# Kernel tuning notes

Measured on AMD Instinct MI355X. Metric: run time of the kernel, lower is better.

Reference implementation:

```python
import jax, jax.numpy as jnp
import numpy as np

H, E, V = 1024, 8, 32000
B, S = 2, 2048
RANK, ALPHA = 4, 1.0
LORA_SCALE = ALPHA / RANK
TOP_K = 2
C1, DEC = 4096, 256
CACHE_SIZES = np.array([C1 - i * DEC for i in range(E)])  # [4096,...,2304]
CMAX = int(CACHE_SIZES.max())
H2 = H // 2  # pyramid compression ratio 0.5


def setup_inputs() -> dict:
    key = jax.random.key(0)
    ks = jax.random.split(key, 24)
    n = lambda k, shape, s=1.0: jax.random.normal(k, shape, dtype=jnp.float32) * s
    w = 1.0 / np.sqrt(H)
    inp = {
        "x": n(ks[0], (B, S, H)),
        "query": n(ks[1], (B, S, H)),
        "cache_values": n(ks[2], (E, CMAX, H)),
        "cache_importance": jax.random.uniform(ks[3], (E, CMAX), dtype=jnp.float32),
        "Wr": n(ks[4], (H, E), w),
        "Wexp": n(ks[5], (E, H, H), w),
        "bexp": jnp.zeros((E, H), jnp.float32),
        "Aexp": n(ks[6], (E, H, RANK), w),
        "Bexp": n(ks[7], (E, RANK, H), w),
        "Wq": n(ks[8], (H, H), w),
        "bq": jnp.zeros((H,), jnp.float32),
        "Wk": n(ks[9], (H, H), w),
        "bk": jnp.zeros((H,), jnp.float32),
        "Aq": n(ks[10], (H, RANK), w),
        "Bq": n(ks[11], (RANK, H), w),
        "Ak": n(ks[12], (H, RANK), w),
        "Bk": n(ks[13], (RANK, H), w),
        "Wd": n(ks[14], (H, H2), w),
        "Wu": n(ks[15], (H2, H), 1.0 / np.sqrt(H2)),
        "Av": n(ks[16], (E, H, RANK), w),
        "Bv": n(ks[17], (E, RANK, H), w),
        "Wv": n(ks[18], (H, V), w),
        "bv": jnp.zeros((V,), jnp.float32),
    }
    # compressor weights are per-expert in the original (one per KVCache)
    inp["Wd"] = n(ks[19], (E, H, H2), w)
    inp["Wu"] = n(ks[20], (E, H2, H), 1.0 / np.sqrt(H2))
    return inp


def reference(x, query, cache_values, cache_importance, Wr, Wexp, bexp, Aexp, Bexp,
              Wq, bq, Wk, bk, Aq, Bq, Ak, Bk, Wd, Wu, Av, Bv, Wv, bv):
    # ---- AdaptiveRouter: softmax gate, top-2, renormalize, scatter to dense ----
    gate = jax.nn.softmax(jnp.einsum("bsh,he->bse", x, Wr), axis=-1)       # [B,S,E]
    topv, topi = jax.lax.top_k(gate, TOP_K)                                 # [B,S,K]
    topv = topv / jnp.sum(topv, axis=-1, keepdims=True)
    rw = jnp.sum(jax.nn.one_hot(topi, E, dtype=x.dtype) * topv[..., None], axis=-2)  # [B,S,E]

    # ---- compute_token_importance: LoRA-augmented q/k projections + attention ----
    q = query @ Wq + bq + LORA_SCALE * ((query @ Aq) @ Bq)                  # [B,S,H]
    k = x @ Wk + bk + LORA_SCALE * ((x @ Ak) @ Bk)                          # [B,S,H]
    att = jax.nn.softmax(jnp.einsum("bqh,bkh->bqk", q, k) / np.sqrt(H), axis=-1)
    importance = jnp.sum(att, axis=1)                                       # [B,S] (sum over queries)

    # ---- per-expert KV cache: pyramid compress (down-gelu-up, importance gate) + value LoRA, masked mean ----
    valid = jnp.asarray(np.arange(CMAX)[None, :] < CACHE_SIZES[:, None], x.dtype)  # [E,Cmax]
    h = jax.nn.gelu(jnp.einsum("ech,ehd->ecd", cache_values, Wd))           # [E,Cmax,H2]
    comp = jnp.einsum("ecd,edh->ech", h, Wu) * jax.nn.sigmoid(cache_importance)[..., None]
    comp = comp + LORA_SCALE * jnp.einsum("ech,ehr,erd->ecd", comp, Av, Bv)
    cached = jnp.sum(comp * valid[..., None], axis=1) / jnp.asarray(CACHE_SIZES, x.dtype)[:, None]  # [E,H]

    # ---- dense loop over all LoRA experts (original runs every expert on every token) ----
    eo = jnp.einsum("bsh,ehd->bsed", x, Wexp) + bexp                        # [B,S,E,H]
    eo = eo + LORA_SCALE * jnp.einsum("bsh,ehr,erd->bsed", x, Aexp, Bexp)
    eo = eo + cached[None, None]                                            # broadcast cached values
    expert_output = jnp.einsum("bsed,bse->bsd", eo, rw)                     # routed combine

    logits = expert_output @ Wv + bv                                        # [B,S,V]
    return logits, importance
```

## Files before the change

### kernel.cpp

```cpp
#include <hip/hip_runtime.h>

typedef __bf16 bf16_t;
typedef __bf16 bf16x4 __attribute__((ext_vector_type(4)));
typedef __bf16 bf16x8 __attribute__((ext_vector_type(8)));
typedef float f32x4 __attribute__((ext_vector_type(4)));

#define AS1 __attribute__((address_space(1)))
#define AS3 __attribute__((address_space(3)))
#define BAR() asm volatile("s_barrier" ::: "memory")

__device__ __forceinline__ void gload_lds16(const void* g, void* l) {
  __builtin_amdgcn_global_load_lds((AS1 void*)g, (AS3 void*)l, 16, 0, 0);
}

__device__ __forceinline__ void stage_tile(const bf16_t* g, int ld, bf16_t* lds, int tid) {
  int w = tid >> 6, lane = tid & 63;
#pragma unroll
  for (int r = 0; r < 2; ++r) {
    int rowbase = r * 64 + w * 16;
    const bf16_t* gp = g + (long)(rowbase + (lane >> 2)) * ld + (lane & 3) * 8;
    bf16_t* lp = lds + rowbase * 32;
    gload_lds16(gp, lp);
  }
}

__device__ __forceinline__ void gemm_core(const bf16_t* A, const bf16_t* Bt, int lda, int ldb,
                                          int K, int rowBase, int colBase,
                                          bf16_t* As, bf16_t* Bs, f32x4 acc[4][4]) {
  int tid = threadIdx.x;
  int lane = tid & 63, w = tid >> 6;
  int wr = w >> 1, wc = w & 1;
  int lr = lane & 15, kg = lane >> 4;
  const bf16_t* Ab = A + (long)rowBase * lda;
  const bf16_t* Bb = Bt + (long)colBase * ldb;
  for (int kt = 0; kt < K; kt += 32) {
    __syncthreads();
    stage_tile(Ab + kt, lda, As, tid);
    stage_tile(Bb + kt, ldb, Bs, tid);
    __syncthreads();
    bf16x8 a[4], b[4];
#pragma unroll
    for (int m = 0; m < 4; ++m)
      a[m] = *(const bf16x8*)&As[(wr * 64 + m * 16 + lr) * 32 + kg * 8];
#pragma unroll
    for (int n = 0; n < 4; ++n)
      b[n] = *(const bf16x8*)&Bs[(wc * 64 + n * 16 + lr) * 32 + kg * 8];
#pragma unroll
    for (int m = 0; m < 4; ++m)
#pragma unroll
      for (int n = 0; n < 4; ++n)
        acc[m][n] = __builtin_amdgcn_mfma_f32_16x16x32_bf16(a[m], b[n], acc[m][n], 0, 0, 0);
  }
}

__device__ __forceinline__ void zero_acc(f32x4 acc[4][4]) {
#pragma unroll
  for (int m = 0; m < 4; ++m)
#pragma unroll
    for (int n = 0; n < 4; ++n)
#pragma unroll
      for (int i = 0; i < 4; ++i) acc[m][n][i] = 0.f;
}

__device__ __forceinline__ void pipe256(const bf16_t* __restrict__ Ag,
                                        const bf16_t* __restrict__ Bg,
                                        int K, int ntk, bf16_t* lds, f32x4 acc[8][4]) {
  int tid = threadIdx.x;
  int lane = tid & 63, w = tid >> 6;
  int wr = w >> 2, wc = w & 3;
  int lr = lane & 15, kg = lane >> 4;
  int colE = ((lane & 7) ^ (lane >> 3)) * 8;
  int r0 = w * 16 + (lane >> 3);

  auto stageA = [&](int t, int h) {
    const bf16_t* g = Ag + (long)(h * 128 + r0) * K + t * 64 + colE;
    bf16_t* l = lds + (t & 1) * 16384 + h * 8192 + w * 1024;
    gload_lds16(g, l);
    gload_lds16(g + (long)8 * K, l + 512);
  };
  auto stageB = [&](int t, int h) {
    const bf16_t* g = Bg + (long)(h * 128 + r0) * K + t * 64 + colE;
    bf16_t* l = lds + 32768 + (t % 3) * 16384 + h * 8192 + w * 1024;
    gload_lds16(g, l);
    gload_lds16(g + (long)8 * K, l + 512);
  };

  stageB(0, 0); stageB(0, 1); stageA(0, 0); stageA(0, 1);
  if (ntk > 1) { stageB(1, 0); stageB(1, 1); }
  if (ntk > 1) asm volatile("s_waitcnt vmcnt(4)" ::: "memory");
  else         asm volatile("s_waitcnt vmcnt(0)" ::: "memory");
  BAR();

  for (int t = 0; t < ntk; ++t) {
    const bf16_t* Ar = lds + (t & 1) * 16384 + wr * 8192;
    const bf16_t* Br = lds + 32768 + (t % 3) * 16384 + (wc >> 1) * 8192;
    int bRowOff = (wc & 1) * 64;
    bf16x8 bfr[4][2];
#pragma unroll
    for (int p = 0; p < 4; ++p) {
      if (p == 0) {
#pragma unroll
        for (int n = 0; n < 4; ++n) {
          int R = bRowOff + n * 16 + lr;
#pragma unroll
          for (int ks = 0; ks < 2; ++ks)
            bfr[n][ks] = *(const bf16x8*)(Br + R * 64 + ((ks * 4 + kg) ^ (R & 7)) * 8);
        }
      }
      bf16x8 afr[2][2];
#pragma unroll
      for (int mm = 0; mm < 2; ++mm) {
        int R = p * 32 + mm * 16 + lr;
#pragma unroll
        for (int ks = 0; ks < 2; ++ks)
          afr[mm][ks] = *(const bf16x8*)(Ar + R * 64 + ((ks * 4 + kg) ^ (R & 7)) * 8);
      }
      if (p < 2) { if (t + 1 < ntk) stageA(t + 1, p); }
      else       { if (t + 2 < ntk) stageB(t + 2, p - 2); }
      BAR();
      asm volatile("s_waitcnt lgkmcnt(0)" ::: "memory");
      __builtin_amdgcn_sched_barrier(0);
      __builtin_amdgcn_s_setprio(1);
#pragma unroll
      for (int mm = 0; mm < 2; ++mm)
#pragma unroll
        for (int n = 0; n < 4; ++n)
#pragma unroll
          for (int ks = 0; ks < 2; ++ks)
            acc[p * 2 + mm][n] =
                __builtin_amdgcn_mfma_f32_16x16x32_bf16(afr[mm][ks], bfr[n][ks],
                                                        acc[p * 2 + mm][n], 0, 0, 0);
      __builtin_amdgcn_s_setprio(0);
      if (p == 3) {
        if (t + 2 < ntk)      asm volatile("s_waitcnt vmcnt(4)" ::: "memory");
        else if (t + 1 < ntk) asm volatile("s_waitcnt vmcnt(0)" ::: "memory");
      }
      BAR();
    }
  }
}

__global__ __launch_bounds__(256) void k_cast(const float* in, bf16_t* out, long n4) {
  long i = (long)blockIdx.x * 256 + threadIdx.x;
  if (i >= n4) return;
  float4 v = ((const float4*)in)[i];
  bf16_t* o = out + i * 4;
  o[0] = (bf16_t)v.x; o[1] = (bf16_t)v.y; o[2] = (bf16_t)v.z; o[3] = (bf16_t)v.w;
}

__global__ __launch_bounds__(256) void k_prep_wt(const float* W, const float* A, const float* Bm,
                                                 bf16_t* out, int K, int N,
                                                 long wstride, long astride, long bstride, long ostride) {
  __shared__ float tile[64][65];
  int e = blockIdx.z;
  W += (long)e * wstride;
  out += (long)e * ostride;
  if (A) { A += (long)e * astride; Bm += (long)e * bstride; }
  int k0 = blockIdx.x * 64, n0 = blockIdx.y * 64;
  int tid = threadIdx.x;
  int tn = tid & 63, tk = tid >> 6;
#pragma unroll 4
  for (int i = 0; i < 16; ++i) {
    int k = tk + i * 4;
    float v = W[(long)(k0 + k) * N + (n0 + tn)];
    if (A) {
      const float* Ak = A + (long)(k0 + k) * 4;
      const float* Bn = Bm + n0 + tn;
      v += 0.25f * (Ak[0] * Bn[0] + Ak[1] * Bn[(long)N] + Ak[2] * Bn[2L * N] + Ak[3] * Bn[3L * N]);
    }
    tile[k][tn] = v;
  }
  __syncthreads();
#pragma unroll 4
  for (int i = 0; i < 16; ++i) {
    int n = tk + i * 4;
    out[(long)(n0 + n) * K + (k0 + tn)] = (bf16_t)tile[tn][n];
  }
}

__global__ __launch_bounds__(256) void k_router(const float* x, const float* Wr, float* rw) {
  int w = threadIdx.x >> 6, lane = threadIdx.x & 63;
  long tok = (long)blockIdx.x * 4 + w;
  const float* xr = x + tok * 1024;
  float acc[8] = {0.f, 0.f, 0.f, 0.f, 0.f, 0.f, 0.f, 0.f};
  for (int h = lane; h < 1024; h += 64) {
    float xv = xr[h];
    const float* wr8 = Wr + h * 8;
#pragma unroll
    for (int e = 0; e < 8; ++e) acc[e] += xv * wr8[e];
  }
#pragma unroll
  for (int o = 32; o; o >>= 1)
#pragma unroll
    for (int e = 0; e < 8; ++e) acc[e] += __shfl_xor(acc[e], o);
  if (lane == 0) {
    int i1 = 0;
    for (int e = 1; e < 8; ++e) if (acc[e] > acc[i1]) i1 = e;
    int i2 = (i1 == 0) ? 1 : 0;
    for (int e = 0; e < 8; ++e) { if (e == i1) continue; if (acc[e] > acc[i2]) i2 = e; }
    float g2 = expf(acc[i2] - acc[i1]);
    float d = 1.f / (1.f + g2);
    float* dst = rw + tok * 8;
#pragma unroll
    for (int e = 0; e < 8; ++e) dst[e] = (e == i1) ? d : ((e == i2) ? g2 * d : 0.f);
  }
}

__global__ __launch_bounds__(256) void k_gemm_bias_bf16(const bf16_t* A, long Az,
                                                        const bf16_t* Bt, long Bz,
                                                        const float* bias0, const float* bias1,
                                                        bf16_t* out, long Oz, int K, int ldc) {
  __shared__ bf16_t As[4096] __attribute__((aligned(16)));
  __shared__ bf16_t Bs[4096] __attribute__((aligned(16)));
  int z = blockIdx.z;
  A += (long)z * Az; Bt += (long)z * Bz; out += (long)z * Oz;
  const float* bias = z ? bias1 : bias0;
  int rowBase = blockIdx.x * 128, colBase = blockIdx.y * 128;
  f32x4 acc[4][4];
  zero_acc(acc);
  gemm_core(A, Bt, K, K, K, rowBase, colBase, As, Bs, acc);
  int tid = threadIdx.x, lane = tid & 63, w = tid >> 6;
  int wr = w >> 1, wc = w & 1, lc = lane & 15, kg = lane >> 4;
#pragma unroll
  for (int m = 0; m < 4; ++m)
#pragma unroll
    for (int n = 0; n < 4; ++n)
#pragma unroll
      for (int r = 0; r < 4; ++r) {
        int gr = rowBase + wr * 64 + m * 16 + kg * 4 + r;
        int gc = colBase + wc * 64 + n * 16 + lc;
        out[(long)gr * ldc + gc] = (bf16_t)(acc[m][n][r] + bias[gc]);
      }
}

template <bool NT>
__global__ __launch_bounds__(256) void k_gemm128(
    const bf16_t* __restrict__ A, long Az, const bf16_t* __restrict__ Bt, long Bz,
    const float* __restrict__ bias, float* __restrict__ out, long Oz,
    int mB, int N, int K, float scale) {
  __shared__ bf16_t As[4096] __attribute__((aligned(16)));
  __shared__ bf16_t Bs[4096] __attribute__((aligned(16)));
  __shared__ float fl[32 * 132];
  int tid = threadIdx.x;
  A += (long)blockIdx.y * Az;
  Bt += (long)blockIdx.y * Bz;
  out += (long)blockIdx.y * Oz;
  int per = gridDim.x >> 3;
  int bid = blockIdx.x;
  int swz = (bid & 7) * per + (bid >> 3);
  int rowB = swz % mB, colB = swz / mB;
  int rowBase = rowB << 7, colBase = colB << 7;
  f32x4 acc[4][4];
  zero_acc(acc);
  gemm_core(A, Bt, K, K, K, rowBase, colBase, As, Bs, acc);
  int lane = tid & 63, w = tid >> 6;
  int wr = w >> 1, wc = w & 1, lc = lane & 15, kg = lane >> 4;
  int colq = (tid & 31) * 4;
  f32x4 bb = {0.f, 0.f, 0.f, 0.f};
  if (bias) bb = *(const f32x4*)(bias + colBase + colq);
#pragma unroll
  for (int c = 0; c < 4; ++c) {
    __syncthreads();
    if (wr == (c >> 1)) {
      int m0 = (c & 1) * 2;
#pragma unroll
      for (int mm = 0; mm < 2; ++mm)
#pragma unroll
        for (int n = 0; n < 4; ++n)
#pragma unroll
          for (int r = 0; r < 4; ++r)
            fl[(mm * 16 + kg * 4 + r) * 132 + wc * 64 + n * 16 + lc] = acc[m0 + mm][n][r] * scale;
    }
    __syncthreads();
    long grow = rowBase + c * 32;
#pragma unroll
    for (int q = 0; q < 4; ++q) {
      int idx = q * 256 + tid;
      int row = idx >> 5;
      f32x4 v = *(const f32x4*)&fl[row * 132 + colq];
      v += bb;
      float* op = out + (grow + row) * (long)N + colBase + colq;
      if (NT) __builtin_nontemporal_store(v, (f32x4*)op);
      else *(f32x4*)op = v;
    }
  }
}

template <bool NT>
__global__ __launch_bounds__(512, 2) void k_gemm256(
    const bf16_t* __restrict__ A, long Az, const bf16_t* __restrict__ Bt, long Bz,
    const float* __restrict__ bias, float* __restrict__ out, long Oz,
    int mBlocks, int N, int K, int ntk, float scale) {
  __shared__ bf16_t lds[81920] __attribute__((aligned(16)));
  int tid = threadIdx.x;
  int lane = tid & 63, w = tid >> 6;
  int wr = w >> 2, wc = w & 3;
  int lr = lane & 15, kg = lane >> 4;
  A += (long)blockIdx.y * Az;
  Bt += (long)blockIdx.y * Bz;
  out += (long)blockIdx.y * Oz;
  int per = gridDim.x >> 3;
  int bid = blockIdx.x;
  int swz = (bid & 7) * per + (bid >> 3);
  int rowB = swz % mBlocks, colB = swz / mBlocks;
  long rowBase = (long)rowB << 8, colBase = (long)colB << 8;

  f32x4 acc[8][4];
#pragma unroll
  for (int m = 0; m < 8; ++m)
#pragma unroll
    for (int n = 0; n < 4; ++n)
#pragma unroll
      for (int i = 0; i < 4; ++i) acc[m][n][i] = 0.f;
  pipe256(A + rowBase * K, Bt + colBase * K, K, ntk, lds, acc);

  float* fl = (float*)lds;
  f32x4 bb4 = {0.f, 0.f, 0.f, 0.f};
  if (bias) bb4 = ((const f32x4*)(bias + colBase))[lane];
#pragma unroll
  for (int c = 0; c < 4; ++c) {
    if ((c >> 1) == wr) {
      int mg0 = (c & 1) * 4;
#pragma unroll
      for (int j = 0; j < 4; ++j)
#pragma unroll
        for (int n = 0; n < 4; ++n) {
          int col = wc * 64 + n * 16 + lr;
          int lrow = j * 16 + kg * 4;
#pragma unroll
          for (int rr = 0; rr < 4; ++rr)
            fl[(lrow + rr) * 260 + col] = acc[mg0 + j][n][rr] * scale;
        }
    }
    BAR();
    long grow = rowBase + c * 64;
#pragma unroll
    for (int q = 0; q < 8; ++q) {
      int r = w * 8 + q;
      f32x4 v = *(const f32x4*)&fl[r * 260 + lane * 4];
      v += bb4;
      float* op = out + (grow + r) * (long)N + colBase + lane * 4;
      if (NT) __builtin_nontemporal_store(v, (f32x4*)op);
      else *(f32x4*)op = v;
    }
    BAR();
  }
}

__global__ __launch_bounds__(512, 2) void k_gemm256h(
    const bf16_t* __restrict__ A, long Az, const bf16_t* __restrict__ Bt, long Bz,
    bf16_t* __restrict__ out, long Oz, int mBlocks, int N, int K, int ntk) {
  __shared__ bf16_t lds[81920] __attribute__((aligned(16)));
  int tid = threadIdx.x;
  int lane = tid & 63, w = tid >> 6;
  int wr = w >> 2, wc = w & 3;
  int lr = lane & 15, kg = lane >> 4;
  A += (long)blockIdx.y * Az;
  Bt += (long)blockIdx.y * Bz;
  out += (long)blockIdx.y * Oz;
  int per = gridDim.x >> 3;
  int bid = blockIdx.x;
  int swz = (bid & 7) * per + (bid >> 3);
  int rowB = swz % mBlocks, colB = swz / mBlocks;
  long rowBase = (long)rowB << 8, colBase = (long)colB << 8;

  f32x4 acc[8][4];
#pragma unroll
  for (int m = 0; m < 8; ++m)
#pragma unroll
    for (int n = 0; n < 4; ++n)
#pragma unroll
      for (int i = 0; i < 4; ++i) acc[m][n][i] = 0.f;
  pipe256(A + rowBase * K, Bt + colBase * K, K, ntk, lds, acc);

  float* fl = (float*)lds;
#pragma unroll
  for (int c = 0; c < 4; ++c) {
    if ((c >> 1) == wr) {
      int mg0 = (c & 1) * 4;
#pragma unroll
      for (int j = 0; j < 4; ++j)
#pragma unroll
        for (int n = 0; n < 4; ++n) {
          int col = wc * 64 + n * 16 + lr;
          int lrow = j * 16 + kg * 4;
#pragma unroll
          for (int rr = 0; rr < 4; ++rr)
            fl[(lrow + rr) * 260 + col] = acc[mg0 + j][n][rr];
        }
    }
    BAR();
    long grow = rowBase + c * 64;
#pragma unroll
    for (int q = 0; q < 8; ++q) {
      int r = w * 8 + q;
      f32x4 v = *(const f32x4*)&fl[r * 260 + lane * 4];
      bf16x4 h;
#pragma unroll
      for (int i = 0; i < 4; ++i) h[i] = (bf16_t)v[i];
      *(bf16x4*)(out + (grow + r) * (long)N + colBase + lane * 4) = h;
    }
    BAR();
  }
}

__global__ __launch_bounds__(512, 2) void k_cache256(
    const bf16_t* __restrict__ cache_bf, const bf16_t* __restrict__ wd_t,
    const float* __restrict__ ci, float* __restrict__ partial) {
  __shared__ bf16_t lds[81920] __attribute__((aligned(16)));
  int tid = threadIdx.x;
  int lane = tid & 63, w = tid >> 6;
  int wr = w >> 2, wc = w & 3;
  int lr = lane & 15, kg = lane >> 4;
  int e = blockIdx.y;
  const bf16_t* A = cache_bf + (long)e * 4194304;
  const bf16_t* Bt = wd_t + (long)e * 524288;
  int per = gridDim.x >> 3;
  int bid = blockIdx.x;
  int swz = (bid & 7) * per + (bid >> 3);
  int rowB = swz % 16, colB = swz / 16;
  long rowBase = (long)rowB << 8, colBase = (long)colB << 8;

  f32x4 acc[8][4];
#pragma unroll
  for (int m = 0; m < 8; ++m)
#pragma unroll
    for (int n = 0; n < 4; ++n)
#pragma unroll
      for (int i = 0; i < 4; ++i) acc[m][n][i] = 0.f;
  pipe256(A + rowBase * 1024, Bt + colBase * 1024, 1024, 16, lds, acc);

  float* colsum = (float*)lds;
  if (tid < 256) colsum[tid] = 0.f;
  __syncthreads();
  int csize = 4096 - 256 * e;
  const float* cie = ci + (long)e * 4096;
  float s[4] = {0.f, 0.f, 0.f, 0.f};
#pragma unroll
  for (int mg = 0; mg < 8; ++mg)
#pragma unroll
    for (int rr = 0; rr < 4; ++rr) {
      int row = (int)rowBase + wr * 128 + mg * 16 + kg * 4 + rr;
      float wf = (row < csize) ? 1.f / (1.f + expf(-cie[row])) : 0.f;
#pragma unroll
      for (int n = 0; n < 4; ++n) {
        float xv = acc[mg][n][rr];
        float t = xv + 0.044715f * xv * xv * xv;
        float gl = 0.5f * xv * (1.f + tanhf(0.7978845608028654f * t));
        s[n] += gl * wf;
      }
    }
#pragma unroll
  for (int n = 0; n < 4; ++n)
    atomicAdd(&colsum[wc * 64 + n * 16 + lr], s[n]);
  __syncthreads();
  if (tid < 256)
    partial[((long)e * 16 + rowB) * 512 + colB * 256 + tid] = colsum[tid];
}

__global__ __launch_bounds__(256) void k_combine(const bf16_t* Y, const float* rw,
                                                 const float* cbc, bf16_t* out) {
  long t = blockIdx.x;
  const float* rwt = rw + t * 8;
  int e1 = -1, e2 = -1;
  float w1 = 0.f, w2 = 0.f;
#pragma unroll
  for (int e = 0; e < 8; ++e) {
    float v = rwt[e];
    if (v > 0.f) { if (e1 < 0) { e1 = e; w1 = v; } else { e2 = e; w2 = v; } }
  }
  if (e1 < 0) { e1 = 0; }
  if (e2 < 0) { e2 = e1; w2 = 0.f; }
  const bf16_t* y1 = Y + ((long)e1 * 4096 + t) * 1024;
  const bf16_t* y2 = Y + ((long)e2 * 4096 + t) * 1024;
  const float* c1 = cbc + e1 * 1024;
  const float* c2 = cbc + e2 * 1024;
  bf16_t* o = out + t * 1024;
  int d = threadIdx.x * 4;
  bf16x4 a = *(const bf16x4*)(y1 + d);
  bf16x4 b = *(const bf16x4*)(y2 + d);
  f32x4 c1v = *(const f32x4*)(c1 + d);
  f32x4 c2v = *(const f32x4*)(c2 + d);
  bf16x4 r;
#pragma unroll
  for (int i = 0; i < 4; ++i)
    r[i] = (bf16_t)(w1 * ((float)a[i] + c1v[i]) + w2 * ((float)b[i] + c2v[i]));
  *(bf16x4*)(o + d) = r;
}

__global__ __launch_bounds__(256) void k_reduce_g(const float* partial, float* g) {
  int e = blockIdx.x, tid = threadIdx.x;
  for (int j = tid; j < 512; j += 256) {
    float s = 0.f;
    for (int mx = 0; mx < 16; ++mx) s += partial[((long)e * 16 + mx) * 512 + j];
    g[e * 512 + j] = s;
  }
}

__global__ __launch_bounds__(256) void k_wu_mv(const float* g, const float* Wu, float* pre) {
  int e = blockIdx.x;
  int d = blockIdx.y * 256 + threadIdx.x;
  __shared__ float gs[512];
  for (int j = threadIdx.x; j < 512; j += 256) gs[j] = g[e * 512 + j];
  __syncthreads();
  const float* W = Wu + (long)e * 524288 + d;
  float s = 0.f;
  for (int j = 0; j < 512; ++j) s += gs[j] * W[(long)j * 1024];
  pre[e * 1024 + d] = s;
}

__global__ __launch_bounds__(256) void k_cached_fin(const float* pre, const float* Av,
                                                    const float* Bv, const float* bexp,
                                                    float* cbc) {
  int e = blockIdx.x, tid = threadIdx.x;
  __shared__ float ps[1024];
  __shared__ float tt[4];
  for (int d = tid; d < 1024; d += 256) ps[d] = pre[e * 1024 + d];
  __syncthreads();
  int w = tid >> 6, lane = tid & 63;
  {
    float s = 0.f;
    const float* Ave = Av + e * 4096;
    for (int d = lane; d < 1024; d += 64) s += ps[d] * Ave[d * 4 + w];
#pragma unroll
    for (int o = 32; o; o >>= 1) s += __shfl_xor(s, o);
    if (lane == 0) tt[w] = s;
  }
  __syncthreads();
  float inv = 1.f / (float)(4096 - 256 * e);
  const float* Bve = Bv + e * 4096;
  for (int d = tid; d < 1024; d += 256) {
    float lora = tt[0] * Bve[d] + tt[1] * Bve[1024 + d] + tt[2] * Bve[2048 + d] + tt[3] * Bve[3072 + d];
    cbc[e * 1024 + d] = (ps[d] + 0.25f * lora) * inv + bexp[e * 1024 + d];
  }
}

__global__ __launch_bounds__(256) void k_rowstat(const float* S, float* mrow, float* zinv) {
  long row = blockIdx.x;
  const float* r = S + row * 2048;
  int tid = threadIdx.x;
  float m = -3.4e38f;
  for (int c = tid; c < 2048; c += 256) m = fmaxf(m, r[c]);
#pragma unroll
  for (int o = 32; o; o >>= 1) m = fmaxf(m, __shfl_xor(m, o));
  __shared__ float sm[4], ss[4];
  if ((tid & 63) == 0) sm[tid >> 6] = m;
  __syncthreads();
  m = fmaxf(fmaxf(sm[0], sm[1]), fmaxf(sm[2], sm[3]));
  float s = 0.f;
  for (int c = tid; c < 2048; c += 256) s += expf(r[c] - m);
#pragma unroll
  for (int o = 32; o; o >>= 1) s += __shfl_xor(s, o);
  if ((tid & 63) == 0) ss[tid >> 6] = s;
  __syncthreads();
  if (tid == 0) { mrow[row] = m; zinv[row] = 1.f / (ss[0] + ss[1] + ss[2] + ss[3]); }
}

__global__ __launch_bounds__(256) void k_imp_part(const float* S, const float* mrow, const float* zinv,
                                                  float* ipart) {
  int k = blockIdx.x * 256 + threadIdx.x;
  int qc = blockIdx.y, b = blockIdx.z;
  const float* Sb = S + (long)b * 4194304;
  const float* mb = mrow + b * 2048;
  const float* zb = zinv + b * 2048;
  float s = 0.f;
  int q0 = qc * 128;
  for (int q = q0; q < q0 + 128; ++q)
    s += expf(Sb[(long)q * 2048 + k] - mb[q]) * zb[q];
  ipart[((long)b * 16 + qc) * 2048 + k] = s;
}

__global__ __launch_bounds__(256) void k_imp_fin(const float* ipart, float* out) {
  int k = blockIdx.x * 256 + threadIdx.x;
  int b = blockIdx.y;
  float s = 0.f;
  for (int qc = 0; qc < 16; ++qc) s += ipart[((long)b * 16 + qc) * 2048 + k];
  out[b * 2048 + k] = s;
}

extern "C" void kernel_launch(void* const* d_in, const int* in_sizes, int n_in,
                              void* d_out, int out_size, void* d_ws, size_t ws_size,
                              hipStream_t stream) {
  (void)in_sizes; (void)n_in; (void)out_size; (void)ws_size;
  const float* x    = (const float*)d_in[0];
  const float* query= (const float*)d_in[1];
  const float* cach = (const float*)d_in[2];
  const float* ci   = (const float*)d_in[3];
  const float* Wr   = (const float*)d_in[4];
  const float* Wexp = (const float*)d_in[5];
  const float* bexp = (const float*)d_in[6];
  const float* Aexp = (const float*)d_in[7];
  const float* Bexp = (const float*)d_in[8];
  const float* Wq   = (const float*)d_in[9];
  const float* bq   = (const float*)d_in[10];
  const float* Wk   = (const float*)d_in[11];
  const float* bk   = (const float*)d_in[12];
  const float* Aq   = (const float*)d_in[13];
  const float* Bq   = (const float*)d_in[14];
  const float* Ak   = (const float*)d_in[15];
  const float* Bk   = (const float*)d_in[16];
  const float* Wd   = (const float*)d_in[17];
  const float* Wu   = (const float*)d_in[18];
  const float* Av   = (const float*)d_in[19];
  const float* Bv   = (const float*)d_in[20];
  const float* Wv   = (const float*)d_in[21];
  const float* bv   = (const float*)d_in[22];
  float* out = (float*)d_out;

  size_t off = 0;
  char* base = (char*)d_ws;
  auto carve = [&](size_t bytes) { char* p = base + off; off = (off + bytes + 255) & ~(size_t)255; return (void*)p; };
  bf16_t* query_bf = (bf16_t*)carve(8388608);
  bf16_t* x_bf     = (bf16_t*)carve(8388608);
  bf16_t* q_bf     = (bf16_t*)carve(8388608);
  bf16_t* k_bf     = (bf16_t*)carve(8388608);
  bf16_t* expert_bf= (bf16_t*)carve(8388608);
  bf16_t* wq_t     = (bf16_t*)carve(2097152);
  bf16_t* wk_t     = (bf16_t*)carve(2097152);
  bf16_t* wd_t     = (bf16_t*)carve(8388608);
  bf16_t* wexp_t   = (bf16_t*)carve(16777216);
  float*  s_att    = (float*)carve(33554432);
  float*  mrow     = (float*)carve(16384);
  float*  zinv     = (float*)carve(16384);
  float*  rw       = (float*)carve(131072);
  float*  partial  = (float*)carve(262144);
  float*  gbuf     = (float*)carve(16384);
  float*  pre      = (float*)carve(32768);
  float*  cbc      = (float*)carve(32768);
  float*  ipart    = (float*)carve(262144);
  void*   uni      = carve(71303168);
  bf16_t* cache_bf = (bf16_t*)uni;
  bf16_t* Y        = (bf16_t*)uni;
  bf16_t* wv_t     = (bf16_t*)uni;

  k_cast<<<4096, 256, 0, stream>>>(x, x_bf, 1048576);
  k_cast<<<4096, 256, 0, stream>>>(query, query_bf, 1048576);
  k_cast<<<32768, 256, 0, stream>>>(cach, cache_bf, 8388608);
  k_prep_wt<<<dim3(16, 16, 1), 256, 0, stream>>>(Wq, Aq, Bq, wq_t, 1024, 1024, 0, 0, 0, 0);
  k_prep_wt<<<dim3(16, 16, 1), 256, 0, stream>>>(Wk, Ak, Bk, wk_t, 1024, 1024, 0, 0, 0, 0);
  k_prep_wt<<<dim3(16, 8, 8), 256, 0, stream>>>(Wd, nullptr, nullptr, wd_t, 1024, 512, 524288, 0, 0, 524288);
  k_prep_wt<<<dim3(16, 16, 8), 256, 0, stream>>>(Wexp, Aexp, Bexp, wexp_t, 1024, 1024, 1048576, 4096, 4096, 1048576);
  k_router<<<1024, 256, 0, stream>>>(x, Wr, rw);
  k_gemm_bias_bf16<<<dim3(32, 8, 2), 256, 0, stream>>>(query_bf, 4194304, wq_t, 1048576,
                                                       bq, bk, q_bf, 4194304, 1024, 1024);
  k_gemm128<false><<<dim3(256, 2), 256, 0, stream>>>(q_bf, 2097152, k_bf, 2097152, nullptr,
                                                     s_att, 4194304, 16, 2048, 1024, 0.03125f);
  k_rowstat<<<4096, 256, 0, stream>>>(s_att, mrow, zinv);
  k_imp_part<<<dim3(8, 16, 2), 256, 0, stream>>>(s_att, mrow, zinv, ipart);
  k_imp_fin<<<dim3(8, 2), 256, 0, stream>>>(ipart, out + 131072000L);
  k_cache256<<<dim3(32, 8), 512, 0, stream>>>(cache_bf, wd_t, ci, partial);
  k_reduce_g<<<8, 256, 0, stream>>>(partial, gbuf);
  k_wu_mv<<<dim3(8, 4), 256, 0, stream>>>(gbuf, Wu, pre);
  k_cached_fin<<<8, 256, 0, stream>>>(pre, Av, Bv, bexp, cbc);
  k_gemm256h<<<dim3(64, 8), 512, 0, stream>>>(x_bf, 0, wexp_t, 1048576, Y, 4194304,
                                              16, 1024, 1024, 16);
  k_combine<<<4096, 256, 0, stream>>>(Y, rw, cbc, expert_bf);
  k_prep_wt<<<dim3(16, 500, 1), 256, 0, stream>>>(Wv, nullptr, nullptr, wv_t, 1024, 32000, 0, 0, 0, 0);
  k_gemm256<true><<<dim3(2000, 1), 512, 0, stream>>>(expert_bf, 0, wv_t, 0, bv,
                                                     out, 0, 16, 32000, 1024, 16, 1.0f);
}
```

Measured before the change: 761.8 us.

## Replace dense all-expert GEMM with routed sparse MoE grouped GEMM

Instead of running every expert on every token and then combining, the new code builds a per-expert token list from the top-2 routing weights and runs a grouped GEMM over 128-row tiles of gathered tokens. The cached bias and routing weight are folded into the epilogue, writing fp32 per-slot outputs that a small kernel sums into bf16. This cuts expert FLOPs by about 4x, at the cost of scheduling kernels, a gathered A-load with a simpler unpipelined GEMM, and fp32 intermediate traffic. It also merges the two input casts, fuses the partial reduction into k_wu_mv, and makes the softmax row-stat kernel single-pass with an online max/sum.

```diff
diff --git a/kernel.cpp b/kernel.cpp
--- a/kernel.cpp
+++ b/kernel.cpp
@@ -144,6 +144,15 @@
   long i = (long)blockIdx.x * 256 + threadIdx.x;
   if (i >= n4) return;
   float4 v = ((const float4*)in)[i];
+  bf16_t* o = out + i * 4;
+  o[0] = (bf16_t)v.x; o[1] = (bf16_t)v.y; o[2] = (bf16_t)v.z; o[3] = (bf16_t)v.w;
+}
+
+__global__ __launch_bounds__(256) void k_cast2(const float* a, const float* b, bf16_t* out) {
+  long i = (long)blockIdx.x * 256 + threadIdx.x;
+  const float* src = (i < 1048576) ? a : b;
+  long j = (i < 1048576) ? i : i - 1048576;
+  float4 v = ((const float4*)src)[j];
   bf16_t* o = out + i * 4;
   o[0] = (bf16_t)v.x; o[1] = (bf16_t)v.y; o[2] = (bf16_t)v.z; o[3] = (bf16_t)v.w;
 }
@@ -204,6 +213,110 @@
 #pragma unroll
     for (int e = 0; e < 8; ++e) dst[e] = (e == i1) ? d : ((e == i2) ? g2 * d : 0.f);
   }
+}
+
+__global__ __launch_bounds__(256) void k_sched(const float* rw, int* eidx, float* ewgt, int* tcnt) {
+  int e = blockIdx.x, tid = threadIdx.x;
+  __shared__ int cnt;
+  if (tid == 0) cnt = 0;
+  __syncthreads();
+  for (int t = tid; t < 4096; t += 256) {
+    const float* r = rw + (long)t * 8;
+    float wv = r[e];
+    if (wv > 0.f) {
+      int slot = 0;
+      for (int j = 0; j < 8; ++j) if (j < e && r[j] > 0.f) slot = 1;
+      int p = atomicAdd(&cnt, 1);
+      eidx[e * 4096 + p] = t * 2 + slot;
+      ewgt[e * 4096 + p] = wv;
+    }
+  }
+  __syncthreads();
+  int c = cnt;
+  int padded = (c + 127) & ~127;
+  for (int p = c + tid; p < padded; p += 256) eidx[e * 4096 + p] = -1;
+  if (tid == 0) tcnt[e] = padded >> 7;
+}
+
+__global__ void k_sched2(const int* tcnt, int* desc, int* ntile) {
+  if (threadIdx.x == 0 && blockIdx.x == 0) {
+    int n = 0;
+    for (int e = 0; e < 8; ++e)
+      for (int i = 0; i < tcnt[e]; ++i) { desc[n * 2] = e; desc[n * 2 + 1] = i; ++n; }
+    *ntile = n;
+  }
+}
+
+__global__ __launch_bounds__(256) void k_moe128(const bf16_t* x_bf, const bf16_t* wexp_t,
+                                                const int* eidx, const float* ewgt,
+                                                const int* desc, const int* ntile,
+                                                const float* cbc, float* Yp) {
+  if ((int)blockIdx.y >= *ntile) return;
+  int e = desc[blockIdx.y * 2], ti = desc[blockIdx.y * 2 + 1];
+  const int* idx = eidx + e * 4096 + ti * 128;
+  const float* wgt = ewgt + e * 4096 + ti * 128;
+  __shared__ bf16_t As[4096] __attribute__((aligned(16)));
+  __shared__ bf16_t Bs[4096] __attribute__((aligned(16)));
+  int tid = threadIdx.x, lane = tid & 63, w = tid >> 6;
+  const bf16_t* aP[2];
+#pragma unroll
+  for (int r = 0; r < 2; ++r) {
+    int row = r * 64 + w * 16 + (lane >> 2);
+    int v = idx[row];
+    int tok = (v < 0) ? 0 : (v >> 1);
+    aP[r] = x_bf + (long)tok * 1024 + (lane & 3) * 8;
+  }
+  const bf16_t* Bb = wexp_t + (long)e * 1048576 + (long)blockIdx.x * 131072;
+  int wr = w >> 1, wc = w & 1, lr = lane & 15, kg = lane >> 4;
+  f32x4 acc[4][4];
+  zero_acc(acc);
+  for (int kt = 0; kt < 1024; kt += 32) {
+    __syncthreads();
+    gload_lds16(aP[0] + kt, As + (w * 16) * 32);
+    gload_lds16(aP[1] + kt, As + (64 + w * 16) * 32);
+    stage_tile(Bb + kt, 1024, Bs, tid);
+    __syncthreads();
+    bf16x8 a[4], b[4];
+#pragma unroll
+    for (int m = 0; m < 4; ++m)
+      a[m] = *(const bf16x8*)&As[(wr * 64 + m * 16 + lr) * 32 + kg * 8];
+#pragma unroll
+    for (int n = 0; n < 4; ++n)
+      b[n] = *(const bf16x8*)&Bs[(wc * 64 + n * 16 + lr) * 32 + kg * 8];
+#pragma unroll
+    for (int m = 0; m < 4; ++m)
+#pragma unroll
+      for (int n = 0; n < 4; ++n)
+        acc[m][n] = __builtin_amdgcn_mfma_f32_16x16x32_bf16(a[m], b[n], acc[m][n], 0, 0, 0);
+  }
+  const float* cb = cbc + e * 1024 + blockIdx.x * 128;
+#pragma unroll
+  for (int m = 0; m < 4; ++m)
+#pragma unroll
+    for (int r = 0; r < 4; ++r) {
+      int lrow = wr * 64 + m * 16 + kg * 4 + r;
+      int v = idx[lrow];
+      if (v < 0) continue;
+      int tok = v >> 1, slot = v & 1;
+      float wg = wgt[lrow];
+      float* op = Yp + ((long)slot * 4096 + tok) * 1024 + blockIdx.x * 128;
+#pragma unroll
+      for (int n = 0; n < 4; ++n) {
+        int gc = wc * 64 + n * 16 + lr;
+        op[gc] = wg * (acc[m][n][r] + cb[gc]);
+      }
+    }
+}
+
+__global__ __launch_bounds__(256) void k_combine2(const float* Yp, bf16_t* out) {
+  long t = blockIdx.x;
+  int d = threadIdx.x * 4;
+  f32x4 a = *(const f32x4*)(Yp + t * 1024 + d);
+  f32x4 b = *(const f32x4*)(Yp + 4194304L + t * 1024 + d);
+  bf16x4 r;
+#pragma unroll
+  for (int i = 0; i < 4; ++i) r[i] = (bf16_t)(a[i] + b[i]);
+  *(bf16x4*)(out + t * 1024 + d) = r;
 }
 
 __global__ __launch_bounds__(256) void k_gemm_bias_bf16(const bf16_t* A, long Az,
@@ -347,63 +460,6 @@
   }
 }
 
-__global__ __launch_bounds__(512, 2) void k_gemm256h(
-    const bf16_t* __restrict__ A, long Az, const bf16_t* __restrict__ Bt, long Bz,
-    bf16_t* __restrict__ out, long Oz, int mBlocks, int N, int K, int ntk) {
-  __shared__ bf16_t lds[81920] __attribute__((aligned(16)));
-  int tid = threadIdx.x;
-  int lane = tid & 63, w = tid >> 6;
-  int wr = w >> 2, wc = w & 3;
-  int lr = lane & 15, kg = lane >> 4;
-  A += (long)blockIdx.y * Az;
-  Bt += (long)blockIdx.y * Bz;
-  out += (long)blockIdx.y * Oz;
-  int per = gridDim.x >> 3;
-  int bid = blockIdx.x;
-  int swz = (bid & 7) * per + (bid >> 3);
-  int rowB = swz % mBlocks, colB = swz / mBlocks;
-  long rowBase = (long)rowB << 8, colBase = (long)colB << 8;
-
-  f32x4 acc[8][4];
-#pragma unroll
-  for (int m = 0; m < 8; ++m)
-#pragma unroll
-    for (int n = 0; n < 4; ++n)
-#pragma unroll
-      for (int i = 0; i < 4; ++i) acc[m][n][i] = 0.f;
-  pipe256(A + rowBase * K, Bt + colBase * K, K, ntk, lds, acc);
-
-  float* fl = (float*)lds;
-#pragma unroll
-  for (int c = 0; c < 4; ++c) {
-    if ((c >> 1) == wr) {
-      int mg0 = (c & 1) * 4;
-#pragma unroll
-      for (int j = 0; j < 4; ++j)
-#pragma unroll
-        for (int n = 0; n < 4; ++n) {
-          int col = wc * 64 + n * 16 + lr;
-          int lrow = j * 16 + kg * 4;
-#pragma unroll
-          for (int rr = 0; rr < 4; ++rr)
-            fl[(lrow + rr) * 260 + col] = acc[mg0 + j][n][rr];
-        }
-    }
-    BAR();
-    long grow = rowBase + c * 64;
-#pragma unroll
-    for (int q = 0; q < 8; ++q) {
-      int r = w * 8 + q;
-      f32x4 v = *(const f32x4*)&fl[r * 260 + lane * 4];
-      bf16x4 h;
-#pragma unroll
-      for (int i = 0; i < 4; ++i) h[i] = (bf16_t)v[i];
-      *(bf16x4*)(out + (grow + r) * (long)N + colBase + lane * 4) = h;
-    }
-    BAR();
-  }
-}
-
 __global__ __launch_bounds__(512, 2) void k_cache256(
     const bf16_t* __restrict__ cache_bf, const bf16_t* __restrict__ wd_t,
     const float* __restrict__ ci, float* __restrict__ partial) {
@@ -458,50 +514,15 @@
     partial[((long)e * 16 + rowB) * 512 + colB * 256 + tid] = colsum[tid];
 }
 
-__global__ __launch_bounds__(256) void k_combine(const bf16_t* Y, const float* rw,
-                                                 const float* cbc, bf16_t* out) {
-  long t = blockIdx.x;
-  const float* rwt = rw + t * 8;
-  int e1 = -1, e2 = -1;
-  float w1 = 0.f, w2 = 0.f;
-#pragma unroll
-  for (int e = 0; e < 8; ++e) {
-    float v = rwt[e];
-    if (v > 0.f) { if (e1 < 0) { e1 = e; w1 = v; } else { e2 = e; w2 = v; } }
-  }
-  if (e1 < 0) { e1 = 0; }
-  if (e2 < 0) { e2 = e1; w2 = 0.f; }
-  const bf16_t* y1 = Y + ((long)e1 * 4096 + t) * 1024;
-  const bf16_t* y2 = Y + ((long)e2 * 4096 + t) * 1024;
-  const float* c1 = cbc + e1 * 1024;
-  const float* c2 = cbc + e2 * 1024;
-  bf16_t* o = out + t * 1024;
-  int d = threadIdx.x * 4;
-  bf16x4 a = *(const bf16x4*)(y1 + d);
-  bf16x4 b = *(const bf16x4*)(y2 + d);
-  f32x4 c1v = *(const f32x4*)(c1 + d);
-  f32x4 c2v = *(const f32x4*)(c2 + d);
-  bf16x4 r;
-#pragma unroll
-  for (int i = 0; i < 4; ++i)
-    r[i] = (bf16_t)(w1 * ((float)a[i] + c1v[i]) + w2 * ((float)b[i] + c2v[i]));
-  *(bf16x4*)(o + d) = r;
-}
-
-__global__ __launch_bounds__(256) void k_reduce_g(const float* partial, float* g) {
-  int e = blockIdx.x, tid = threadIdx.x;
-  for (int j = tid; j < 512; j += 256) {
-    float s = 0.f;
-    for (int mx = 0; mx < 16; ++mx) s += partial[((long)e * 16 + mx) * 512 + j];
-    g[e * 512 + j] = s;
-  }
-}
-
-__global__ __launch_bounds__(256) void k_wu_mv(const float* g, const float* Wu, float* pre) {
+__global__ __launch_bounds__(256) void k_wu_mv(const float* partial, const float* Wu, float* pre) {
   int e = blockIdx.x;
   int d = blockIdx.y * 256 + threadIdx.x;
   __shared__ float gs[512];
-  for (int j = threadIdx.x; j < 512; j += 256) gs[j] = g[e * 512 + j];
+  for (int j = threadIdx.x; j < 512; j += 256) {
+    float s = 0.f;
+    for (int mx = 0; mx < 16; ++mx) s += partial[((long)e * 16 + mx) * 512 + j];
+    gs[j] = s;
+  }
   __syncthreads();
   const float* W = Wu + (long)e * 524288 + d;
   float s = 0.f;
@@ -539,21 +560,29 @@
   long row = blockIdx.x;
   const float* r = S + row * 2048;
   int tid = threadIdx.x;
-  float m = -3.4e38f;
-  for (int c = tid; c < 2048; c += 256) m = fmaxf(m, r[c]);
-#pragma unroll
-  for (int o = 32; o; o >>= 1) m = fmaxf(m, __shfl_xor(m, o));
+  float m = -3.4e38f, s = 0.f;
+  for (int c = tid; c < 2048; c += 256) {
+    float v = r[c];
+    if (v > m) { s = s * expf(m - v) + 1.f; m = v; }
+    else s += expf(v - m);
+  }
+#pragma unroll
+  for (int o = 32; o; o >>= 1) {
+    float mo = __shfl_xor(m, o), so = __shfl_xor(s, o);
+    float M = fmaxf(m, mo);
+    s = s * expf(m - M) + so * expf(mo - M);
+    m = M;
+  }
   __shared__ float sm[4], ss[4];
-  if ((tid & 63) == 0) sm[tid >> 6] = m;
-  __syncthreads();
-  m = fmaxf(fmaxf(sm[0], sm[1]), fmaxf(sm[2], sm[3]));
-  float s = 0.f;
-  for (int c = tid; c < 2048; c += 256) s += expf(r[c] - m);
-#pragma unroll
-  for (int o = 32; o; o >>= 1) s += __shfl_xor(s, o);
-  if ((tid & 63) == 0) ss[tid >> 6] = s;
-  __syncthreads();
-  if (tid == 0) { mrow[row] = m; zinv[row] = 1.f / (ss[0] + ss[1] + ss[2] + ss[3]); }
+  if ((tid & 63) == 0) { sm[tid >> 6] = m; ss[tid >> 6] = s; }
+  __syncthreads();
+  if (tid == 0) {
+    float M = fmaxf(fmaxf(sm[0], sm[1]), fmaxf(sm[2], sm[3]));
+    float S2 = ss[0] * expf(sm[0] - M) + ss[1] * expf(sm[1] - M) +
+               ss[2] * expf(sm[2] - M) + ss[3] * expf(sm[3] - M);
+    mrow[row] = M;
+    zinv[row] = 1.f / S2;
+  }
 }
 
 __global__ __launch_bounds__(256) void k_imp_part(const float* S, const float* mrow, const float* zinv,
@@ -624,23 +653,28 @@
   float*  zinv     = (float*)carve(16384);
   float*  rw       = (float*)carve(131072);
   float*  partial  = (float*)carve(262144);
-  float*  gbuf     = (float*)carve(16384);
   float*  pre      = (float*)carve(32768);
   float*  cbc      = (float*)carve(32768);
   float*  ipart    = (float*)carve(262144);
+  int*    eidx     = (int*)carve(131072);
+  float*  ewgt     = (float*)carve(131072);
+  int*    tcnt     = (int*)carve(256);
+  int*    desc     = (int*)carve(1024);
+  int*    ntile    = (int*)carve(256);
   void*   uni      = carve(71303168);
   bf16_t* cache_bf = (bf16_t*)uni;
-  bf16_t* Y        = (bf16_t*)uni;
+  float*  Yp       = (float*)uni;
   bf16_t* wv_t     = (bf16_t*)uni;
 
-  k_cast<<<4096, 256, 0, stream>>>(x, x_bf, 1048576);
-  k_cast<<<4096, 256, 0, stream>>>(query, query_bf, 1048576);
+  k_cast2<<<8192, 256, 0, stream>>>(query, x, query_bf);
   k_cast<<<32768, 256, 0, stream>>>(cach, cache_bf, 8388608);
   k_prep_wt<<<dim3(16, 16, 1), 256, 0, stream>>>(Wq, Aq, Bq, wq_t, 1024, 1024, 0, 0, 0, 0);
   k_prep_wt<<<dim3(16, 16, 1), 256, 0, stream>>>(Wk, Ak, Bk, wk_t, 1024, 1024, 0, 0, 0, 0);
   k_prep_wt<<<dim3(16, 8, 8), 256, 0, stream>>>(Wd, nullptr, nullptr, wd_t, 1024, 512, 524288, 0, 0, 524288);
   k_prep_wt<<<dim3(16, 16, 8), 256, 0, stream>>>(Wexp, Aexp, Bexp, wexp_t, 1024, 1024, 1048576, 4096, 4096, 1048576);
   k_router<<<1024, 256, 0, stream>>>(x, Wr, rw);
+  k_sched<<<8, 256, 0, stream>>>(rw, eidx, ewgt, tcnt);
+  k_sched2<<<1, 64, 0, stream>>>(tcnt, desc, ntile);
   k_gemm_bias_bf16<<<dim3(32, 8, 2), 256, 0, stream>>>(query_bf, 4194304, wq_t, 1048576,
                                                        bq, bk, q_bf, 4194304, 1024, 1024);
   k_gemm128<false><<<dim3(256, 2), 256, 0, stream>>>(q_bf, 2097152, k_bf, 2097152, nullptr,
@@ -649,12 +683,10 @@
   k_imp_part<<<dim3(8, 16, 2), 256, 0, stream>>>(s_att, mrow, zinv, ipart);
   k_imp_fin<<<dim3(8, 2), 256, 0, stream>>>(ipart, out + 131072000L);
   k_cache256<<<dim3(32, 8), 512, 0, stream>>>(cache_bf, wd_t, ci, partial);
-  k_reduce_g<<<8, 256, 0, stream>>>(partial, gbuf);
-  k_wu_mv<<<dim3(8, 4), 256, 0, stream>>>(gbuf, Wu, pre);
+  k_wu_mv<<<dim3(8, 4), 256, 0, stream>>>(partial, Wu, pre);
   k_cached_fin<<<8, 256, 0, stream>>>(pre, Av, Bv, bexp, cbc);
-  k_gemm256h<<<dim3(64, 8), 512, 0, stream>>>(x_bf, 0, wexp_t, 1048576, Y, 4194304,
-                                              16, 1024, 1024, 16);
-  k_combine<<<4096, 256, 0, stream>>>(Y, rw, cbc, expert_bf);
+  k_moe128<<<dim3(8, 72), 256, 0, stream>>>(x_bf, wexp_t, eidx, ewgt, desc, ntile, cbc, Yp);
+  k_combine2<<<4096, 256, 0, stream>>>(Yp, expert_bf);
   k_prep_wt<<<dim3(16, 500, 1), 256, 0, stream>>>(Wv, nullptr, nullptr, wv_t, 1024, 32000, 0, 0, 0, 0);
   k_gemm256<true><<<dim3(2000, 1), 512, 0, stream>>>(expert_bf, 0, wv_t, 0, bv,
                                                      out, 0, 16, 32000, 1024, 16, 1.0f);
```

Result: no change. 765.8 us (+0.5%).
